# Kernel optimization log

Hardware: AMD Instinct MI355X
Metric: run time of the kernel (lower is better)

Reference implementation:

```python
import jax, jax.numpy as jnp
import numpy as np

N = 100000      # nodes
E = 1600000     # edges
FX = 128        # raw node feature dim
MAXZ = 100      # z embedding / one-hot size
HID = 128       # hidden_channels
NL = 3          # num_layers
G = 512         # num graphs
BN_EPS = 1e-5


def _lin(key, din, dout):
    return jax.random.normal(key, (din, dout), jnp.float32) * (1.0 / np.sqrt(din))


def setup_inputs() -> dict:
    key = jax.random.key(0)
    ks = jax.random.split(key, 64)
    d = {}
    d["x"] = jax.random.normal(ks[0], (N, FX), jnp.float32)
    d["z"] = jax.random.randint(ks[1], (N,), 0, MAXZ)
    d["edge_index"] = jax.random.randint(ks[2], (2, E), 0, N)
    d["batch"] = jnp.sort(jax.random.randint(ks[3], (N,), 0, G))
    in0 = FX + 2 * MAXZ  # z_emb concatenated twice (faithful to source)
    ki = 4
    for l in range(NL):
        din = in0 if l == 0 else HID
        d[f"W1_{l}"] = _lin(ks[ki], din, HID); ki += 1
        d[f"b1_{l}"] = jnp.zeros((HID,), jnp.float32)
        d[f"W2_{l}"] = _lin(ks[ki], HID, HID); ki += 1
        d[f"b2_{l}"] = jnp.zeros((HID,), jnp.float32)
        d[f"g_{l}"] = jnp.ones((HID,), jnp.float32)
        d[f"be_{l}"] = jnp.zeros((HID,), jnp.float32)
    d["Wl1"] = _lin(ks[ki], NL * HID, HID); ki += 1
    d["bl1"] = jnp.zeros((HID,), jnp.float32)
    d["Wl2"] = _lin(ks[ki], HID, 1); ki += 1
    d["bl2"] = jnp.zeros((1,), jnp.float32)
    return d


def _gin_layer(h, src, dst, W1, b1, W2, b2, g, be):
    # GINConv with eps=0: nn(x + sum_{j->i} x_j)
    agg = jax.ops.segment_sum(h[src], dst, num_segments=N)  # [N, d]
    m = h + agg
    m = jax.nn.relu(m @ W1 + b1)
    m = jax.nn.relu(m @ W2 + b2)
    # training-mode BatchNorm1d over node axis (biased variance)
    mu = m.mean(0)
    var = jnp.mean((m - mu) ** 2, axis=0)
    return (m - mu) * jax.lax.rsqrt(var + BN_EPS) * g + be


def reference(x, z, edge_index, batch,
              W1_0, b1_0, W2_0, b2_0, g_0, be_0,
              W1_1, b1_1, W2_1, b2_1, g_1, be_1,
              W1_2, b1_2, W2_2, b2_2, g_2, be_2,
              Wl1, bl1, Wl2, bl2):
    src, dst = edge_index[0], edge_index[1]
    z_emb = jax.nn.one_hot(z, MAXZ, dtype=jnp.float32)  # [N, MAXZ]
    h = jnp.concatenate([z_emb, x], axis=1)
    h = jnp.concatenate([z_emb, h], axis=1)  # faithful double concat -> [N, FX+2*MAXZ]
    params = [(W1_0, b1_0, W2_0, b2_0, g_0, be_0),
              (W1_1, b1_1, W2_1, b2_1, g_1, be_1),
              (W1_2, b1_2, W2_2, b2_2, g_2, be_2)]
    xs = []
    for p in params:
        h = _gin_layer(h, src, dst, *p)
        xs.append(h)
    hcat = jnp.concatenate(xs, axis=1)  # jumping knowledge: [N, NL*HID]
    # global_mean_pool over graph ids
    counts = jax.ops.segment_sum(jnp.ones((N,), jnp.float32), batch, num_segments=G)
    pooled = jax.ops.segment_sum(hcat, batch, num_segments=G) / jnp.maximum(counts, 1.0)[:, None]
    out = jax.nn.relu(pooled @ Wl1 + bl1)
    # dropout is identity in eval / reference mode
    out = out @ Wl2 + bl2  # [G, 1]
    return out
```

## Files before the change

kernel.cpp:

```cpp
#include <hip/hip_runtime.h>
#include <hip/hip_bf16.h>

#define NN 100000
#define NROWS_PAD 100032
#define EE 1600000
#define GG 512
#define NPB 256
#define NB  ((NN + NPB - 1) / NPB)
#define PCHUNK 4096
#define PBLOCKS ((EE + PCHUNK - 1) / PCHUNK)
#define SBANK 8
static constexpr float BN_EPS = 1e-5f;

typedef _Float16 half8 __attribute__((ext_vector_type(8)));
typedef float floatx4 __attribute__((ext_vector_type(4)));


__global__ __launch_bounds__(256) void k_bhist(const int* __restrict__ EI,
                                               int* __restrict__ bcount)
{
    __shared__ int h[NB];
    const int t = threadIdx.x;
    for (int i = t; i < NB; i += 256) h[i] = 0;
    __syncthreads();
    const int e0 = blockIdx.x * PCHUNK;
    const int e1 = (e0 + PCHUNK < EE) ? e0 + PCHUNK : EE;
    for (int e = e0 + t; e < e1; e += 256)
        atomicAdd(&h[EI[EE + e] >> 8], 1);
    __syncthreads();
    for (int i = t; i < NB; i += 256)
        if (h[i]) atomicAdd(&bcount[i], h[i]);
}

__global__ __launch_bounds__(512) void k_bscan(const int* __restrict__ bcount,
                                               int* __restrict__ bstart,
                                               int* __restrict__ bcursor,
                                               int* __restrict__ row_start)
{
    __shared__ int s[512];
    int t = threadIdx.x;
    int v = (t < NB) ? bcount[t] : 0;
    s[t] = v;
    __syncthreads();
    for (int off = 1; off < 512; off <<= 1) {
        int u = (t >= off) ? s[t - off] : 0;
        __syncthreads();
        s[t] += u;
        __syncthreads();
    }
    if (t < NB) { int ex = s[t] - v; bstart[t] = ex; bcursor[t] = ex; }
    if (t == 0) { bstart[NB] = EE; row_start[NN] = EE; }
}

__global__ __launch_bounds__(256) void k_part(const int* __restrict__ EI,
                                              int* __restrict__ bcursor,
                                              int* __restrict__ ebuf)
{
    __shared__ int h[NB];
    __shared__ int cur[NB];
    const int t = threadIdx.x;
    for (int i = t; i < NB; i += 256) h[i] = 0;
    __syncthreads();
    const int e0 = blockIdx.x * PCHUNK;
    const int e1 = (e0 + PCHUNK < EE) ? e0 + PCHUNK : EE;
    for (int e = e0 + t; e < e1; e += 256)
        atomicAdd(&h[EI[EE + e] >> 8], 1);
    __syncthreads();
    for (int i = t; i < NB; i += 256)
        cur[i] = h[i] ? atomicAdd(&bcursor[i], h[i]) : 0;
    __syncthreads();
    for (int e = e0 + t; e < e1; e += 256) {
        int s = EI[e], d = EI[EE + e];
        int pos = atomicAdd(&cur[d >> 8], 1);
        ebuf[pos] = s | ((d & (NPB - 1)) << 17);
    }
}

__global__ __launch_bounds__(256) void k_csrbucket(const int* __restrict__ ebuf,
                                                   const int* __restrict__ bstart,
                                                   int* __restrict__ row_start,
                                                   int* __restrict__ ssrc)
{
    __shared__ int cnt[NPB];
    __shared__ int cur[NPB];
    const int b = blockIdx.x, t = threadIdx.x;
    cnt[t] = 0;
    __syncthreads();
    const int e0 = bstart[b], e1 = bstart[b + 1];
    for (int e = e0 + t; e < e1; e += 256) {
        unsigned p = (unsigned)__builtin_nontemporal_load(&ebuf[e]);
        atomicAdd(&cnt[p >> 17], 1);
    }
    __syncthreads();
    int myc = cnt[t];
    for (int off = 1; off < 256; off <<= 1) {
        int u = (t >= off) ? cnt[t - off] : 0;
        __syncthreads();
        cnt[t] += u;
        __syncthreads();
    }
    int pos0 = e0 + cnt[t] - myc;
    int idx = b * NPB + t;
    if (idx < NN) row_start[idx] = pos0;
    cur[t] = pos0;
    __syncthreads();
    for (int e = e0 + t; e < e1; e += 256) {
        unsigned p = (unsigned)__builtin_nontemporal_load(&ebuf[e]);
        int pos = atomicAdd(&cur[p >> 17], 1);
        ssrc[pos] = (int)(p & 0x1FFFFu);
    }
}


__global__ __launch_bounds__(256) void k_xcast(const float* __restrict__ X,
                                               _Float16* __restrict__ Xh)
{
    int idx = blockIdx.x * 256 + threadIdx.x;
    const float4* src = (const float4*)X;
    float4 a = src[idx * 2], b = src[idx * 2 + 1];
    half8 o = { (_Float16)a.x, (_Float16)a.y, (_Float16)a.z, (_Float16)a.w,
                (_Float16)b.x, (_Float16)b.y, (_Float16)b.z, (_Float16)b.w };
    *(half8*)&Xh[idx * 8] = o;
}

__device__ __forceinline__ void bn_sc_sh(const float* statsL,
                                         const float* g, const float* be, int k,
                                         float& sc, float& sh)
{
    float cs = 0.f, cq = 0.f;
    #pragma unroll
    for (int b = 0; b < SBANK; ++b) {
        cs += statsL[b * 256 + k];
        cq += statsL[b * 256 + 128 + k];
    }
    float inv_n = 1.0f / (float)NN;
    float mu = cs * inv_n;
    float var = cq * inv_n - mu * mu;
    sc = g[k] * rsqrtf(var + BN_EPS);
    sh = be[k] - mu * sc;
}

__global__ __launch_bounds__(256) void k_prep(
    const float* __restrict__ W1, const float* __restrict__ W2,
    const float* __restrict__ statsPrev,
    const float* __restrict__ g, const float* __restrict__ be,
    _Float16* __restrict__ Wt1, _Float16* __restrict__ Wt2,
    float* __restrict__ cvec, int l)
{
    int b = blockIdx.x, t = threadIdx.x;
    if (b < 64) {
        int idx = b * 256 + t;
        int n = idx >> 7, k = idx & 127;
        if (l == 0) {
            Wt1[idx] = (_Float16)W1[(200 + k) * 128 + n];
        } else {
            float sc, sh;
            bn_sc_sh(statsPrev, g, be, k, sc, sh);
            Wt1[idx] = (_Float16)(sc * W1[k * 128 + n]);
        }
    } else if (b < 128) {
        int idx = (b - 64) * 256 + t;
        int n = idx >> 7, k = idx & 127;
        Wt2[idx] = (_Float16)W2[k * 128 + n];
    } else if (t < 128) {
        float acc = 0.f;
        if (l != 0) {
            for (int k = 0; k < 128; ++k) {
                float sc, sh;
                bn_sc_sh(statsPrev, g, be, k, sc, sh);
                acc = fmaf(sh, W1[k * 128 + t], acc);
            }
        }
        cvec[t] = acc;
    }
}


#define MM_CORE_G(Ah, Wth)                                                   \
    const int lane = tid & 63;                                               \
    const int wv = tid >> 6;                                                 \
    const int ml = lane & 15;                                                \
    const int quad = lane >> 4;                                              \
    const int wr = wv >> 1, wc = wv & 1;                                     \
    floatx4 acc[2][4];                                                       \
    for (int r = 0; r < 2; ++r)                                              \
        for (int t = 0; t < 4; ++t)                                          \
            acc[r][t] = (floatx4){0.f, 0.f, 0.f, 0.f};                       \
    {                                                                        \
        const size_t ar0 = (size_t)(row0 + 32 * wr + ml) * 128;              \
        const size_t ar1 = ar0 + (size_t)16 * 128;                           \
        _Pragma("unroll")                                                    \
        for (int kq = 0; kq < 4; ++kq) {                                     \
            int k0 = kq * 32;                                                \
            half8 a0 = *(const half8*)&Ah[ar0 + k0 + quad * 8];              \
            half8 a1 = *(const half8*)&Ah[ar1 + k0 + quad * 8];              \
            _Pragma("unroll")                                                \
            for (int t = 0; t < 4; ++t) {                                    \
                half8 bf = *(const half8*)&Wth[(size_t)(64 * wc + 16 * t + ml) * 128 + k0 + quad * 8]; \
                acc[0][t] = __builtin_amdgcn_mfma_f32_16x16x32_f16(a0, bf, acc[0][t], 0, 0, 0); \
                acc[1][t] = __builtin_amdgcn_mfma_f32_16x16x32_f16(a1, bf, acc[1][t], 0, 0, 0); \
            }                                                                \
        }                                                                    \
    }

__global__ __launch_bounds__(256) void k_mm_embed(
    const _Float16* __restrict__ Ah, const _Float16* __restrict__ Wth,
    const int* __restrict__ Z, const float* __restrict__ W1,
    _Float16* __restrict__ Ph)
{
    const int tid = threadIdx.x;
    const int row0 = blockIdx.x * 64;
    MM_CORE_G(Ah, Wth)
    #pragma unroll
    for (int r = 0; r < 2; ++r)
        #pragma unroll
        for (int j = 0; j < 4; ++j) {
            int grow = row0 + 32 * wr + 16 * r + quad * 4 + j;
            if (grow < NN) {
                int zv = Z[grow];
                const float* w0 = &W1[zv * 128];
                const float* w1 = &W1[(100 + zv) * 128];
                #pragma unroll
                for (int t = 0; t < 4; ++t) {
                    int gcol = 64 * wc + 16 * t + ml;
                    float v = acc[r][t][j] + w0[gcol] + w1[gcol];
                    Ph[(size_t)grow * 128 + gcol] = (_Float16)v;
                }
            }
        }
}

__global__ __launch_bounds__(256) void k_mm1(
    const _Float16* __restrict__ Ah, const _Float16* __restrict__ Wth,
    _Float16* __restrict__ Ph)
{
    const int tid = threadIdx.x;
    const int row0 = blockIdx.x * 64;
    MM_CORE_G(Ah, Wth)
    #pragma unroll
    for (int r = 0; r < 2; ++r)
        #pragma unroll
        for (int j = 0; j < 4; ++j) {
            int grow = row0 + 32 * wr + 16 * r + quad * 4 + j;
            if (grow < NN) {
                #pragma unroll
                for (int t = 0; t < 4; ++t) {
                    int gcol = 64 * wc + 16 * t + ml;
                    Ph[(size_t)grow * 128 + gcol] = (_Float16)acc[r][t][j];
                }
            }
        }
}

__global__ __launch_bounds__(256) void k_mm2(
    const _Float16* __restrict__ Ah, const _Float16* __restrict__ Wth,
    const float* __restrict__ b2, _Float16* __restrict__ Oh,
    float* __restrict__ statsL)
{
    __shared__ float cs[128];
    __shared__ float cq[128];
    const int tid = threadIdx.x;
    const int row0 = blockIdx.x * 64;
    if (tid < 128) { cs[tid] = 0.f; cq[tid] = 0.f; }
    __syncthreads();

    MM_CORE_G(Ah, Wth)

    float b2v[4];
    #pragma unroll
    for (int t = 0; t < 4; ++t) b2v[t] = b2[64 * wc + 16 * t + ml];
    float st[4] = {0.f, 0.f, 0.f, 0.f};
    float qt[4] = {0.f, 0.f, 0.f, 0.f};
    #pragma unroll
    for (int r = 0; r < 2; ++r)
        #pragma unroll
        for (int j = 0; j < 4; ++j) {
            int grow = row0 + 32 * wr + 16 * r + quad * 4 + j;
            if (grow < NN) {
                #pragma unroll
                for (int t = 0; t < 4; ++t) {
                    int gcol = 64 * wc + 16 * t + ml;
                    float v = fmaxf(acc[r][t][j] + b2v[t], 0.f);
                    Oh[(size_t)grow * 128 + gcol] = (_Float16)v;
                    st[t] += v;
                    qt[t] += v * v;
                }
            }
        }
    #pragma unroll
    for (int t = 0; t < 4; ++t) {
        int gcol = 64 * wc + 16 * t + ml;
        atomicAdd(&cs[gcol], st[t]);
        atomicAdd(&cq[gcol], qt[t]);
    }
    __syncthreads();
    if (tid < 128) {
        float* bank = statsL + (blockIdx.x & (SBANK - 1)) * 256;
        atomicAdd(&bank[tid], cs[tid]);
        atomicAdd(&bank[128 + tid], cq[tid]);
    }
}


__global__ __launch_bounds__(256) void k_aggregate(
    const _Float16* __restrict__ Ph, const int* __restrict__ row_start,
    const int* __restrict__ ssrc, const float* __restrict__ b1,
    const float* __restrict__ cvec, _Float16* __restrict__ Mh)
{
    int idx = blockIdx.x * 256 + threadIdx.x;
    int node = idx >> 4, q = idx & 15;
    if (node >= NN) return;
    int s0 = row_start[node], s1 = row_start[node + 1];
    float degp1 = (float)(s1 - s0 + 1);
    float acc[8];
    half8 pv = *(const half8*)&Ph[(size_t)node * 128 + q * 8];
    #pragma unroll
    for (int j = 0; j < 8; ++j)
        acc[j] = (float)pv[j] + fmaf(degp1, cvec[q * 8 + j], b1[q * 8 + j]);
    int e = s0;
    for (; e + 7 < s1; e += 8) {
        int sidx[8];
        #pragma unroll
        for (int u = 0; u < 8; ++u)
            sidx[u] = __builtin_nontemporal_load(&ssrc[e + u]);
        half8 v[8];
        #pragma unroll
        for (int u = 0; u < 8; ++u)
            v[u] = *(const half8*)&Ph[(size_t)sidx[u] * 128 + q * 8];
        #pragma unroll
        for (int j = 0; j < 8; ++j)
            acc[j] += (((float)v[0][j] + (float)v[1][j]) + ((float)v[2][j] + (float)v[3][j]))
                    + (((float)v[4][j] + (float)v[5][j]) + ((float)v[6][j] + (float)v[7][j]));
    }
    for (; e + 1 < s1; e += 2) {
        int sa = __builtin_nontemporal_load(&ssrc[e]);
        int sb = __builtin_nontemporal_load(&ssrc[e + 1]);
        half8 va = *(const half8*)&Ph[(size_t)sa * 128 + q * 8];
        half8 vb = *(const half8*)&Ph[(size_t)sb * 128 + q * 8];
        #pragma unroll
        for (int j = 0; j < 8; ++j) acc[j] += (float)va[j] + (float)vb[j];
    }
    if (e < s1) {
        int sa = __builtin_nontemporal_load(&ssrc[e]);
        half8 va = *(const half8*)&Ph[(size_t)sa * 128 + q * 8];
        #pragma unroll
        for (int j = 0; j < 8; ++j) acc[j] += (float)va[j];
    }
    half8 o;
    #pragma unroll
    for (int j = 0; j < 8; ++j) o[j] = (_Float16)fmaxf(acc[j], 0.f);
    __builtin_nontemporal_store(o, (half8*)&Mh[(size_t)node * 128 + q * 8]);
}


__global__ __launch_bounds__(128) void k_pool(
    const _Float16* __restrict__ Ah, const int* __restrict__ batch,
    const float* __restrict__ statsL,
    const float* __restrict__ g_, const float* __restrict__ be,
    float* __restrict__ pooled, int loff)
{
    __shared__ float red[8][128];
    int g = blockIdx.x;
    int t = threadIdx.x;
    int rg = t >> 4, seg = t & 15;
    int lo = 0, hi = NN;
    while (lo < hi) { int mid = (lo + hi) >> 1; if (batch[mid] < g) lo = mid + 1; else hi = mid; }
    int s = lo;
    lo = s; hi = NN;
    while (lo < hi) { int mid = (lo + hi) >> 1; if (batch[mid] < g + 1) lo = mid + 1; else hi = mid; }
    int e = lo;
    float acc[8] = {};
    for (int i = s + rg; i < e; i += 8) {
        half8 v = *(const half8*)&Ah[(size_t)i * 128 + seg * 8];
        #pragma unroll
        for (int j = 0; j < 8; ++j) acc[j] += (float)v[j];
    }
    #pragma unroll
    for (int j = 0; j < 8; ++j) red[rg][seg * 8 + j] = acc[j];
    __syncthreads();
    int cnt = e - s;
    float inv = 1.0f / (float)(cnt > 0 ? cnt : 1);
    if (t < 128) {
        float s_ = 0.f;
        #pragma unroll
        for (int r = 0; r < 8; ++r) s_ += red[r][t];
        float sc, sh;
        bn_sc_sh(statsL, g_, be, t, sc, sh);
        pooled[g * 384 + loff + t] = fmaf(sc, s_ * inv, sh);
    }
}

__global__ __launch_bounds__(128) void k_final(
    const float* __restrict__ pooled,
    const float* __restrict__ Wl1, const float* __restrict__ bl1,
    const float* __restrict__ Wl2, const float* __restrict__ bl2,
    float* __restrict__ out)
{
    __shared__ float pr[384];
    __shared__ float red[128];
    int g = blockIdx.x, j = threadIdx.x;
    for (int i = j; i < 384; i += 128) pr[i] = pooled[g * 384 + i];
    __syncthreads();
    float acc = bl1[j];
    for (int k = 0; k < 384; ++k) acc = fmaf(pr[k], Wl1[k * 128 + j], acc);
    float r = fmaxf(acc, 0.f) * Wl2[j];
    red[j] = r;
    __syncthreads();
    for (int off = 64; off > 0; off >>= 1) {
        if (j < off) red[j] += red[j + off];
        __syncthreads();
    }
    if (j == 0) out[g] = red[0] + bl2[0];
}

extern "C" void kernel_launch(void* const* d_in, const int* in_sizes, int n_in,
                              void* d_out, int out_size, void* d_ws, size_t ws_size,
                              hipStream_t stream)
{
    const float* x     = (const float*)d_in[0];
    const int*   z     = (const int*)d_in[1];
    const int*   ei    = (const int*)d_in[2];
    const int*   batch = (const int*)d_in[3];
    const float* W1a[3] = {(const float*)d_in[4],  (const float*)d_in[10], (const float*)d_in[16]};
    const float* b1a[3] = {(const float*)d_in[5],  (const float*)d_in[11], (const float*)d_in[17]};
    const float* W2a[3] = {(const float*)d_in[6],  (const float*)d_in[12], (const float*)d_in[18]};
    const float* b2a[3] = {(const float*)d_in[7],  (const float*)d_in[13], (const float*)d_in[19]};
    const float* ga[3]  = {(const float*)d_in[8],  (const float*)d_in[14], (const float*)d_in[20]};
    const float* bea[3] = {(const float*)d_in[9],  (const float*)d_in[15], (const float*)d_in[21]};
    const float* Wl1 = (const float*)d_in[22];
    const float* bl1 = (const float*)d_in[23];
    const float* Wl2 = (const float*)d_in[24];
    const float* bl2 = (const float*)d_in[25];
    float* out = (float*)d_out;

    char* ws = (char*)d_ws;
    size_t off = 0;
    auto alloc = [&](size_t bytes) {
        void* p = ws + off;
        off += (bytes + 255) & ~(size_t)255;
        return p;
    };
    _Float16* Xh  = (_Float16*)alloc((size_t)NROWS_PAD * 128 * 2);
    _Float16* Ph  = (_Float16*)alloc((size_t)NROWS_PAD * 128 * 2);
    _Float16* Mh  = (_Float16*)alloc((size_t)NROWS_PAD * 128 * 2);
    _Float16* Ahb = (_Float16*)alloc((size_t)NROWS_PAD * 128 * 2);
    _Float16* Wt1 = (_Float16*)alloc((size_t)128 * 128 * 2);
    _Float16* Wt2 = (_Float16*)alloc((size_t)128 * 128 * 2);
    int*   ebuf     = (int*)alloc((size_t)EE * 4);
    int*   ssrc     = (int*)alloc((size_t)EE * 4);
    int*   row_st   = (int*)alloc((size_t)(NN + 1) * 4);
    int*   bcount   = (int*)alloc((size_t)NB * 4);
    int*   bstart   = (int*)alloc((size_t)(NB + 1) * 4);
    int*   bcursor  = (int*)alloc((size_t)NB * 4);
    float* cvec     = (float*)alloc(128 * 4);
    float* stats    = (float*)alloc((size_t)3 * SBANK * 256 * 4);
    float* pooled   = (float*)alloc((size_t)GG * 384 * 4);

    const int gemmBlocks = (NN + 63) / 64;
    const int aggBlocks  = (NN * 16 + 255) / 256;

    hipMemsetAsync(stats, 0, (size_t)3 * SBANK * 256 * 4, stream);
    hipMemsetAsync(bcount, 0, (size_t)NB * 4, stream);
    k_xcast<<<(NN * 128 / 8 + 255) / 256, 256, 0, stream>>>(x, Xh);
    k_bhist<<<PBLOCKS, 256, 0, stream>>>(ei, bcount);
    k_bscan<<<1, 512, 0, stream>>>(bcount, bstart, bcursor, row_st);
    k_part<<<PBLOCKS, 256, 0, stream>>>(ei, bcursor, ebuf);
    k_csrbucket<<<NB, 256, 0, stream>>>(ebuf, bstart, row_st, ssrc);

    for (int l = 0; l < 3; ++l) {
        float* statsL   = stats + (size_t)l * SBANK * 256;
        const float* statsPrev = (l > 0) ? stats + (size_t)(l - 1) * SBANK * 256 : stats;
        const float* pg   = (l > 0) ? ga[l - 1] : ga[0];
        const float* pbe  = (l > 0) ? bea[l - 1] : bea[0];
        k_prep<<<129, 256, 0, stream>>>(W1a[l], W2a[l], statsPrev, pg, pbe,
                                        Wt1, Wt2, cvec, l);
        if (l == 0)
            k_mm_embed<<<gemmBlocks, 256, 0, stream>>>(Xh, Wt1, z, W1a[0], Ph);
        else
            k_mm1<<<gemmBlocks, 256, 0, stream>>>(Ahb, Wt1, Ph);
        k_aggregate<<<aggBlocks, 256, 0, stream>>>(Ph, row_st, ssrc, b1a[l], cvec, Mh);
        k_mm2<<<gemmBlocks, 256, 0, stream>>>(Mh, Wt2, b2a[l], Ahb, statsL);
        k_pool<<<GG, 128, 0, stream>>>(Ahb, batch, statsL, ga[l], bea[l],
                                       pooled, l * 128);
    }
    k_final<<<GG, 128, 0, stream>>>(pooled, Wl1, bl1, Wl2, bl2, out);
}
```

Measured before the change: 706.5 us.

## Fuse x fp16 cast into embed GEMM, stage GEMM outputs via LDS, widen pool

```diff
diff --git a/kernel.cpp b/kernel.cpp
--- a/kernel.cpp
+++ b/kernel.cpp
@@ -111,17 +111,6 @@
     }
 }
 
-
-__global__ __launch_bounds__(256) void k_xcast(const float* __restrict__ X,
-                                               _Float16* __restrict__ Xh)
-{
-    int idx = blockIdx.x * 256 + threadIdx.x;
-    const float4* src = (const float4*)X;
-    float4 a = src[idx * 2], b = src[idx * 2 + 1];
-    half8 o = { (_Float16)a.x, (_Float16)a.y, (_Float16)a.z, (_Float16)a.w,
-                (_Float16)b.x, (_Float16)b.y, (_Float16)b.z, (_Float16)b.w };
-    *(half8*)&Xh[idx * 8] = o;
-}
 
 __device__ __forceinline__ void bn_sc_sh(const float* statsL,
                                          const float* g, const float* be, int k,
@@ -203,11 +192,81 @@
         }                                                                    \
     }
 
+#define MM_STORE_LDS(Csh, Out)                                               \
+    __syncthreads();                                                         \
+    _Pragma("unroll")                                                        \
+    for (int c = 0; c < 4; ++c) {                                            \
+        int chunk = tid * 8 + c * 2048;                                      \
+        if (row0 + (chunk >> 7) < NN)                                        \
+            *(half8*)&Out[(size_t)row0 * 128 + chunk] = *(const half8*)&Csh[chunk]; \
+    }
+
 __global__ __launch_bounds__(256) void k_mm_embed(
-    const _Float16* __restrict__ Ah, const _Float16* __restrict__ Wth,
+    const float* __restrict__ X, const _Float16* __restrict__ Wth,
     const int* __restrict__ Z, const float* __restrict__ W1,
     _Float16* __restrict__ Ph)
 {
+    __shared__ _Float16 Csh[64 * 128];
+    const int tid = threadIdx.x;
+    const int row0 = blockIdx.x * 64;
+    const int lane = tid & 63;
+    const int wv = tid >> 6;
+    const int ml = lane & 15;
+    const int quad = lane >> 4;
+    const int wr = wv >> 1, wc = wv & 1;
+    floatx4 acc[2][4];
+    #pragma unroll
+    for (int r = 0; r < 2; ++r)
+        #pragma unroll
+        for (int t = 0; t < 4; ++t)
+            acc[r][t] = (floatx4){0.f, 0.f, 0.f, 0.f};
+    int r0g = row0 + 32 * wr + ml;
+    int r1g = r0g + 16;
+    if (r0g > NN - 1) r0g = NN - 1;
+    if (r1g > NN - 1) r1g = NN - 1;
+    const float* x0 = &X[(size_t)r0g * 128];
+    const float* x1 = &X[(size_t)r1g * 128];
+    #pragma unroll
+    for (int kq = 0; kq < 4; ++kq) {
+        int k0 = kq * 32 + quad * 8;
+        float4 f0a = *(const float4*)&x0[k0];
+        float4 f0b = *(const float4*)&x0[k0 + 4];
+        float4 f1a = *(const float4*)&x1[k0];
+        float4 f1b = *(const float4*)&x1[k0 + 4];
+        half8 a0 = { (_Float16)f0a.x, (_Float16)f0a.y, (_Float16)f0a.z, (_Float16)f0a.w,
+                     (_Float16)f0b.x, (_Float16)f0b.y, (_Float16)f0b.z, (_Float16)f0b.w };
+        half8 a1 = { (_Float16)f1a.x, (_Float16)f1a.y, (_Float16)f1a.z, (_Float16)f1a.w,
+                     (_Float16)f1b.x, (_Float16)f1b.y, (_Float16)f1b.z, (_Float16)f1b.w };
+        #pragma unroll
+        for (int t = 0; t < 4; ++t) {
+            half8 bf = *(const half8*)&Wth[(size_t)(64 * wc + 16 * t + ml) * 128 + kq * 32 + quad * 8];
+            acc[0][t] = __builtin_amdgcn_mfma_f32_16x16x32_f16(a0, bf, acc[0][t], 0, 0, 0);
+            acc[1][t] = __builtin_amdgcn_mfma_f32_16x16x32_f16(a1, bf, acc[1][t], 0, 0, 0);
+        }
+    }
+    #pragma unroll
+    for (int r = 0; r < 2; ++r)
+        #pragma unroll
+        for (int j = 0; j < 4; ++j) {
+            int lrow = 32 * wr + 16 * r + quad * 4 + j;
+            int grow = row0 + lrow;
+            int zv = (grow < NN) ? Z[grow] : 0;
+            const float* w0 = &W1[zv * 128];
+            const float* w1 = &W1[(100 + zv) * 128];
+            #pragma unroll
+            for (int t = 0; t < 4; ++t) {
+                int gcol = 64 * wc + 16 * t + ml;
+                Csh[lrow * 128 + gcol] = (_Float16)(acc[r][t][j] + w0[gcol] + w1[gcol]);
+            }
+        }
+    MM_STORE_LDS(Csh, Ph)
+}
+
+__global__ __launch_bounds__(256) void k_mm1(
+    const _Float16* __restrict__ Ah, const _Float16* __restrict__ Wth,
+    _Float16* __restrict__ Ph)
+{
+    __shared__ _Float16 Csh[64 * 128];
     const int tid = threadIdx.x;
     const int row0 = blockIdx.x * 64;
     MM_CORE_G(Ah, Wth)
@@ -215,41 +274,12 @@
     for (int r = 0; r < 2; ++r)
         #pragma unroll
         for (int j = 0; j < 4; ++j) {
-            int grow = row0 + 32 * wr + 16 * r + quad * 4 + j;
-            if (grow < NN) {
-                int zv = Z[grow];
-                const float* w0 = &W1[zv * 128];
-                const float* w1 = &W1[(100 + zv) * 128];
-                #pragma unroll
-                for (int t = 0; t < 4; ++t) {
-                    int gcol = 64 * wc + 16 * t + ml;
-                    float v = acc[r][t][j] + w0[gcol] + w1[gcol];
-                    Ph[(size_t)grow * 128 + gcol] = (_Float16)v;
-                }
-            }
+            int lrow = 32 * wr + 16 * r + quad * 4 + j;
+            #pragma unroll
+            for (int t = 0; t < 4; ++t)
+                Csh[lrow * 128 + 64 * wc + 16 * t + ml] = (_Float16)acc[r][t][j];
         }
-}
-
-__global__ __launch_bounds__(256) void k_mm1(
-    const _Float16* __restrict__ Ah, const _Float16* __restrict__ Wth,
-    _Float16* __restrict__ Ph)
-{
-    const int tid = threadIdx.x;
-    const int row0 = blockIdx.x * 64;
-    MM_CORE_G(Ah, Wth)
-    #pragma unroll
-    for (int r = 0; r < 2; ++r)
-        #pragma unroll
-        for (int j = 0; j < 4; ++j) {
-            int grow = row0 + 32 * wr + 16 * r + quad * 4 + j;
-            if (grow < NN) {
-                #pragma unroll
-                for (int t = 0; t < 4; ++t) {
-                    int gcol = 64 * wc + 16 * t + ml;
-                    Ph[(size_t)grow * 128 + gcol] = (_Float16)acc[r][t][j];
-                }
-            }
-        }
+    MM_STORE_LDS(Csh, Ph)
 }
 
 __global__ __launch_bounds__(256) void k_mm2(
@@ -257,6 +287,7 @@
     const float* __restrict__ b2, _Float16* __restrict__ Oh,
     float* __restrict__ statsL)
 {
+    __shared__ _Float16 Csh[64 * 128];
     __shared__ float cs[128];
     __shared__ float cq[128];
     const int tid = threadIdx.x;
@@ -275,16 +306,15 @@
     for (int r = 0; r < 2; ++r)
         #pragma unroll
         for (int j = 0; j < 4; ++j) {
-            int grow = row0 + 32 * wr + 16 * r + quad * 4 + j;
-            if (grow < NN) {
-                #pragma unroll
-                for (int t = 0; t < 4; ++t) {
-                    int gcol = 64 * wc + 16 * t + ml;
-                    float v = fmaxf(acc[r][t][j] + b2v[t], 0.f);
-                    Oh[(size_t)grow * 128 + gcol] = (_Float16)v;
-                    st[t] += v;
-                    qt[t] += v * v;
-                }
+            int lrow = 32 * wr + 16 * r + quad * 4 + j;
+            bool ok = (row0 + lrow) < NN;
+            #pragma unroll
+            for (int t = 0; t < 4; ++t) {
+                int gcol = 64 * wc + 16 * t + ml;
+                float v = ok ? fmaxf(acc[r][t][j] + b2v[t], 0.f) : 0.f;
+                Csh[lrow * 128 + gcol] = (_Float16)v;
+                st[t] += v;
+                qt[t] += v * v;
             }
         }
     #pragma unroll
@@ -293,7 +323,7 @@
         atomicAdd(&cs[gcol], st[t]);
         atomicAdd(&cq[gcol], qt[t]);
     }
-    __syncthreads();
+    MM_STORE_LDS(Csh, Oh)
     if (tid < 128) {
         float* bank = statsL + (blockIdx.x & (SBANK - 1)) * 256;
         atomicAdd(&bank[tid], cs[tid]);
@@ -353,13 +383,13 @@
 }
 
 
-__global__ __launch_bounds__(128) void k_pool(
+__global__ __launch_bounds__(256) void k_pool(
     const _Float16* __restrict__ Ah, const int* __restrict__ batch,
     const float* __restrict__ statsL,
     const float* __restrict__ g_, const float* __restrict__ be,
     float* __restrict__ pooled, int loff)
 {
-    __shared__ float red[8][128];
+    __shared__ float red[16][128];
     int g = blockIdx.x;
     int t = threadIdx.x;
     int rg = t >> 4, seg = t & 15;
@@ -370,7 +400,7 @@
     while (lo < hi) { int mid = (lo + hi) >> 1; if (batch[mid] < g + 1) lo = mid + 1; else hi = mid; }
     int e = lo;
     float acc[8] = {};
-    for (int i = s + rg; i < e; i += 8) {
+    for (int i = s + rg; i < e; i += 16) {
         half8 v = *(const half8*)&Ah[(size_t)i * 128 + seg * 8];
         #pragma unroll
         for (int j = 0; j < 8; ++j) acc[j] += (float)v[j];
@@ -383,7 +413,7 @@
     if (t < 128) {
         float s_ = 0.f;
         #pragma unroll
-        for (int r = 0; r < 8; ++r) s_ += red[r][t];
+        for (int r = 0; r < 16; ++r) s_ += red[r][t];
         float sc, sh;
         bn_sc_sh(statsL, g_, be, t, sc, sh);
         pooled[g * 384 + loff + t] = fmaf(sc, s_ * inv, sh);
@@ -440,7 +470,6 @@
         off += (bytes + 255) & ~(size_t)255;
         return p;
     };
-    _Float16* Xh  = (_Float16*)alloc((size_t)NROWS_PAD * 128 * 2);
     _Float16* Ph  = (_Float16*)alloc((size_t)NROWS_PAD * 128 * 2);
     _Float16* Mh  = (_Float16*)alloc((size_t)NROWS_PAD * 128 * 2);
     _Float16* Ahb = (_Float16*)alloc((size_t)NROWS_PAD * 128 * 2);
@@ -461,7 +490,6 @@
 
     hipMemsetAsync(stats, 0, (size_t)3 * SBANK * 256 * 4, stream);
     hipMemsetAsync(bcount, 0, (size_t)NB * 4, stream);
-    k_xcast<<<(NN * 128 / 8 + 255) / 256, 256, 0, stream>>>(x, Xh);
     k_bhist<<<PBLOCKS, 256, 0, stream>>>(ei, bcount);
     k_bscan<<<1, 512, 0, stream>>>(bcount, bstart, bcursor, row_st);
     k_part<<<PBLOCKS, 256, 0, stream>>>(ei, bcursor, ebuf);
@@ -475,12 +503,12 @@
         k_prep<<<129, 256, 0, stream>>>(W1a[l], W2a[l], statsPrev, pg, pbe,
                                         Wt1, Wt2, cvec, l);
         if (l == 0)
-            k_mm_embed<<<gemmBlocks, 256, 0, stream>>>(Xh, Wt1, z, W1a[0], Ph);
+            k_mm_embed<<<gemmBlocks, 256, 0, stream>>>(x, Wt1, z, W1a[0], Ph);
         else
             k_mm1<<<gemmBlocks, 256, 0, stream>>>(Ahb, Wt1, Ph);
         k_aggregate<<<aggBlocks, 256, 0, stream>>>(Ph, row_st, ssrc, b1a[l], cvec, Mh);
         k_mm2<<<gemmBlocks, 256, 0, stream>>>(Mh, Wt2, b2a[l], Ahb, statsL);
-        k_pool<<<GG, 128, 0, stream>>>(Ahb, batch, statsL, ga[l], bea[l],
+        k_pool<<<GG, 256, 0, stream>>>(Ahb, batch, statsL, ga[l], bea[l],
                                        pooled, l * 128);
     }
     k_final<<<GG, 128, 0, stream>>>(pooled, Wl1, bl1, Wl2, bl2, out);
```

Result: faster. 651.8 us (-7.7%).
